# Kernel optimization log

Hardware: AMD Instinct MI355X
Metric: run time of the kernel (lower is better)

Reference implementation:

```python
import jax, jax.numpy as jnp
import numpy as np

B, S, D = 4, 2048, 1024
H = 16
HD = D // H

def setup_inputs() -> dict:
    key = jax.random.key(0)
    ks = jax.random.split(key, 6)
    scale = 0.02
    return {
        "x": jax.random.normal(ks[0], (B, S, D), dtype=jnp.float32),
        "W_q": jax.random.normal(ks[1], (D, D), dtype=jnp.float32) * scale,
        "W_k": jax.random.normal(ks[2], (D, D), dtype=jnp.float32) * scale,
        "W_v": jax.random.normal(ks[3], (D, D), dtype=jnp.float32) * scale,
        "W_o": jax.random.normal(ks[4], (D, D), dtype=jnp.float32) * scale,
        "b_o": jax.random.normal(ks[5], (D,), dtype=jnp.float32) * scale,
    }

def reference(x, W_q, W_k, W_v, W_o, b_o):
    b, s, d = x.shape
    # projections, split heads: [b, h, s, hd]
    q = (x @ W_q).reshape(b, s, H, HD).transpose(0, 2, 1, 3)
    k = (x @ W_k).reshape(b, s, H, HD).transpose(0, 2, 1, 3)
    v = (x @ W_v).reshape(b, s, H, HD).transpose(0, 2, 1, 3)
    scores = jnp.einsum('bhqd,bhkd->bhqk', q, k)
    causal = jnp.triu(jnp.ones((s, s), dtype=bool), k=1)
    scores = jnp.where(causal, -jnp.inf, scores)
    # module divides by sqrt(hd) after masking; -inf stays -inf
    attn = jax.nn.softmax(scores / jnp.sqrt(jnp.float32(HD)), axis=-1)
    ctx = jnp.einsum('bhqk,bhkd->bhqd', attn, v)
    ctx = ctx.transpose(0, 2, 1, 3).reshape(b, s, d)
    return ctx @ W_o + b_o
```

## Files before the change

### kernel.cpp

```cpp
#include <hip/hip_runtime.h>
#include <hip/hip_bf16.h>
#include <math.h>

typedef __attribute__((ext_vector_type(8))) short bf16x8;
typedef __attribute__((ext_vector_type(4))) float f32x4;
typedef unsigned short u16;
typedef __hip_bfloat16 HB;

#define B_ 4
#define S_ 2048
#define D_ 1024
#define H_ 16
#define HD_ 64

__device__ __forceinline__ u16 f2b(float f) {
  HB h = __float2bfloat16(f);
  return *reinterpret_cast<u16*>(&h);
}
__device__ __forceinline__ void store1(HB* p, float v) { *p = __float2bfloat16(v); }
__device__ __forceinline__ void store1(float* p, float v) { *p = v; }

__device__ __forceinline__ void glds16(const u16* g, u16* l) {
  __builtin_amdgcn_global_load_lds(
      (const __attribute__((address_space(1))) void*)g,
      (__attribute__((address_space(3))) void*)l, 16, 0, 0);
}

__global__ __launch_bounds__(256) void cast_x(const float* __restrict__ xin,
                                              u16* __restrict__ xout) {
  const long i0 = ((long)blockIdx.x * 256 + threadIdx.x) * 8;
  bf16x8 r;
#pragma unroll
  for (int j = 0; j < 8; ++j) r[j] = (short)f2b(xin[i0 + j]);
  *(bf16x8*)(xout + i0) = r;
}

__global__ __launch_bounds__(256) void transpose_w(
    const float* __restrict__ w0, const float* __restrict__ w1,
    const float* __restrict__ w2, const float* __restrict__ w3,
    u16* __restrict__ out) {
  __shared__ __align__(16) u16 T[64 * 72];
  const float* Ws[4] = {w0, w1, w2, w3};
  const float* W = Ws[blockIdx.z];
  u16* Wt = out + (long)blockIdx.z * (1 << 20);
  const int t = threadIdx.x;
  const int r = t >> 3;
  const int c8 = (t & 7) * 8;
#pragma unroll
  for (int it = 0; it < 2; ++it) {
    const int row = blockIdx.y * 64 + it * 32 + r;
    const float* src = W + (long)row * D_ + blockIdx.x * 64 + c8;
#pragma unroll
    for (int j = 0; j < 8; ++j) T[(c8 + j) * 72 + it * 32 + r] = f2b(src[j]);
  }
  __syncthreads();
#pragma unroll
  for (int it = 0; it < 2; ++it) {
    const int row = it * 32 + r;
    bf16x8 v = *(const bf16x8*)(&T[row * 72 + c8]);
    *(bf16x8*)(Wt + (long)(blockIdx.x * 64 + row) * D_ + blockIdx.y * 64 + c8) = v;
  }
}

template <typename OT>
__global__ __launch_bounds__(256) void gemm_bt128(
    const u16* __restrict__ A, const u16* __restrict__ BTb, long bt_stride,
    OT* __restrict__ Cb, long c_stride, const float* __restrict__ bias,
    u16* __restrict__ vt, int scale_q, int M, int N, int K) {
  const u16* BT = BTb + (long)blockIdx.z * bt_stride;
  OT* C = Cb + (long)blockIdx.z * c_stride;

  __shared__ __align__(16) u16 As[128 * 32];
  __shared__ __align__(16) u16 Bs[128 * 32];

  const int tid = threadIdx.x;
  const int w = tid >> 6, lane = tid & 63;
  const int qr = lane & 15, quad = lane >> 4;
  const int wm = w >> 1, wn = w & 1;

  const long rowA0 = (long)blockIdx.y * 128;
  const long rowB0 = (long)blockIdx.x * 128;

  const int sr = lane >> 2;
  const int sc8 = ((lane & 3) ^ ((lane >> 3) & 3)) * 8;
  const long arow = rowA0 + w * 16 + sr;
  const long brow = rowB0 + w * 16 + sr;
  u16* asd0 = As + (w * 16) * 32;
  u16* asd1 = As + (64 + w * 16) * 32;
  u16* bsd0 = Bs + (w * 16) * 32;
  u16* bsd1 = Bs + (64 + w * 16) * 32;

  f32x4 acc[4][4] = {};

  for (int k0 = 0; k0 < K; k0 += 32) {
    __syncthreads();
    glds16(A + arow * K + k0 + sc8, asd0);
    glds16(A + (arow + 64) * K + k0 + sc8, asd1);
    glds16(BT + brow * K + k0 + sc8, bsd0);
    glds16(BT + (brow + 64) * K + k0 + sc8, bsd1);
    __syncthreads();

    bf16x8 af[4], bf[4];
#pragma unroll
    for (int ms = 0; ms < 4; ++ms) {
      const int m = wm * 64 + ms * 16 + qr;
      af[ms] = *(const bf16x8*)(&As[m * 32 + ((quad ^ ((m >> 1) & 3)) * 8)]);
    }
#pragma unroll
    for (int ns = 0; ns < 4; ++ns) {
      const int n = wn * 64 + ns * 16 + qr;
      bf[ns] = *(const bf16x8*)(&Bs[n * 32 + ((quad ^ ((n >> 1) & 3)) * 8)]);
    }

#pragma unroll
    for (int ms = 0; ms < 4; ++ms)
#pragma unroll
      for (int ns = 0; ns < 4; ++ns)
        acc[ms][ns] = __builtin_amdgcn_mfma_f32_16x16x32_bf16(
            af[ms], bf[ns], acc[ms][ns], 0, 0, 0);
  }

  if (vt && blockIdx.z == 2) {
#pragma unroll
    for (int ns = 0; ns < 4; ++ns) {
      const int col = (int)rowB0 + wn * 64 + ns * 16 + qr;
#pragma unroll
      for (int ms = 0; ms < 4; ++ms) {
        const long row = rowA0 + wm * 64 + ms * 16 + quad * 4;
        const long b = row >> 11, s = row & 2047;
        ushort4 pk;
        pk.x = f2b(acc[ms][ns][0]); pk.y = f2b(acc[ms][ns][1]);
        pk.z = f2b(acc[ms][ns][2]); pk.w = f2b(acc[ms][ns][3]);
        *(ushort4*)(vt + ((b * H_ + (col >> 6)) * HD_ + (col & 63)) * S_ + s) = pk;
      }
    }
    return;
  }

  const float qs = (scale_q && blockIdx.z == 0) ? 0.125f : 1.f;
#pragma unroll
  for (int ns = 0; ns < 4; ++ns) {
    const long col = rowB0 + wn * 64 + ns * 16 + qr;
    const float bv = bias ? bias[col] : 0.f;
#pragma unroll
    for (int ms = 0; ms < 4; ++ms) {
      const long row = rowA0 + wm * 64 + ms * 16 + quad * 4;
#pragma unroll
      for (int r = 0; r < 4; ++r)
        store1(&C[(row + r) * (long)N + col], acc[ms][ns][r] * qs + bv);
    }
  }
}

__global__ __launch_bounds__(256) void attn4(
    const u16* __restrict__ Q, const u16* __restrict__ Kg,
    const u16* __restrict__ Vt, u16* __restrict__ ctx) {
  __shared__ __align__(16) u16 KV[2][2][64 * 64];
  __shared__ __align__(16) u16 Pl[4][2][16 * 72];

  const int tid = threadIdx.x;
  const int w = tid >> 6, lane = tid & 63;
  const int qr = lane & 15, quad = lane >> 4;
  const int bh = blockIdx.x;
  const int b = bh >> 4, h = bh & 15;

  const long baseQK = ((long)b * S_) * D_ + h * HD_;
  const long baseVt = (long)bh * HD_ * S_;

  const int sr8 = lane >> 3;
  const int sc8 = ((lane & 7) ^ sr8) * 8;

  const int tiles2[2] = {(int)blockIdx.y, 15 - (int)blockIdx.y};

#pragma unroll
  for (int ti = 0; ti < 2; ++ti) {
    const int q0 = tiles2[ti] * 128;
    const int qbase = q0 + w * 32;

    bf16x8 aq[2][2];
#pragma unroll
    for (int i = 0; i < 2; ++i) {
      const u16* qp_ = Q + baseQK + (long)(qbase + i * 16 + qr) * D_;
      aq[i][0] = *(const bf16x8*)(qp_ + quad * 8);
      aq[i][1] = *(const bf16x8*)(qp_ + 32 + quad * 8);
    }

    float l_i[2][4] = {};
    f32x4 o[2][4] = {};

    const int nkt = q0 / 64 + 2;

#pragma unroll
    for (int t = 0; t < 2; ++t) {
      const int r = t * 32 + w * 8 + sr8;
      glds16(Kg + baseQK + (long)r * D_ + sc8, &KV[0][0][(t * 32 + w * 8) * 64]);
      glds16(Vt + baseVt + (long)r * S_ + sc8, &KV[0][1][(t * 32 + w * 8) * 64]);
    }

    for (int kt = 0; kt < nkt; ++kt) {
      const int kbase = kt * 64;
      const int buf = kt & 1;

      __syncthreads();

      if (kt + 1 < nkt) {
        const int nb = kbase + 64;
#pragma unroll
        for (int t = 0; t < 2; ++t) {
          const int r = t * 32 + w * 8 + sr8;
          glds16(Kg + baseQK + (long)(nb + r) * D_ + sc8,
                 &KV[buf ^ 1][0][(t * 32 + w * 8) * 64]);
          glds16(Vt + baseVt + (long)r * S_ + nb + sc8,
                 &KV[buf ^ 1][1][(t * 32 + w * 8) * 64]);
        }
      }

      const u16* Ksb = KV[buf][0];
      const u16* Vsb = KV[buf][1];

      bf16x8 kf[4][2];
#pragma unroll
      for (int ns = 0; ns < 4; ++ns) {
        const int row = ns * 16 + qr;
        kf[ns][0] = *(const bf16x8*)(&Ksb[row * 64 + ((quad ^ (row & 7)) * 8)]);
        kf[ns][1] =
            *(const bf16x8*)(&Ksb[row * 64 + (((4 + quad) ^ (row & 7)) * 8)]);
      }

      f32x4 s[2][4] = {};
#pragma unroll
      for (int i = 0; i < 2; ++i)
#pragma unroll
        for (int ns = 0; ns < 4; ++ns) {
          s[i][ns] = __builtin_amdgcn_mfma_f32_16x16x32_bf16(
              aq[i][0], kf[ns][0], s[i][ns], 0, 0, 0);
          s[i][ns] = __builtin_amdgcn_mfma_f32_16x16x32_bf16(
              aq[i][1], kf[ns][1], s[i][ns], 0, 0, 0);
        }

#pragma unroll
      for (int i = 0; i < 2; ++i) {
        if (kbase + 64 > qbase + i * 16) {
          const int qrow = qbase + i * 16 + quad * 4;
#pragma unroll
          for (int ns = 0; ns < 4; ++ns) {
            const int kcol = kbase + ns * 16 + qr;
#pragma unroll
            for (int r = 0; r < 4; ++r)
              if (kcol > qrow + r) s[i][ns][r] = -1.0e30f;
          }
        }
      }

#pragma unroll
      for (int i = 0; i < 2; ++i) {
        float psum[4] = {};
#pragma unroll
        for (int ns = 0; ns < 4; ++ns)
#pragma unroll
          for (int r = 0; r < 4; ++r) {
            const float p = __expf(s[i][ns][r]);
            psum[r] += p;
            Pl[w][i][(quad * 4 + r) * 72 + ns * 16 + qr] = f2b(p);
          }
#pragma unroll
        for (int r = 0; r < 4; ++r) {
          float ps = psum[r];
#pragma unroll
          for (int off = 1; off < 16; off <<= 1) ps += __shfl_xor(ps, off, 64);
          l_i[i][r] += ps;
        }
      }

      bf16x8 vf[4][2];
#pragma unroll
      for (int ns = 0; ns < 4; ++ns) {
        const int row = ns * 16 + qr;
        vf[ns][0] = *(const bf16x8*)(&Vsb[row * 64 + ((quad ^ (row & 7)) * 8)]);
        vf[ns][1] =
            *(const bf16x8*)(&Vsb[row * 64 + (((4 + quad) ^ (row & 7)) * 8)]);
      }

#pragma unroll
      for (int i = 0; i < 2; ++i) {
        bf16x8 pf0 = *(const bf16x8*)(&Pl[w][i][qr * 72 + quad * 8]);
        bf16x8 pf1 = *(const bf16x8*)(&Pl[w][i][qr * 72 + 32 + quad * 8]);
#pragma unroll
        for (int ns = 0; ns < 4; ++ns) {
          o[i][ns] = __builtin_amdgcn_mfma_f32_16x16x32_bf16(pf0, vf[ns][0],
                                                             o[i][ns], 0, 0, 0);
          o[i][ns] = __builtin_amdgcn_mfma_f32_16x16x32_bf16(pf1, vf[ns][1],
                                                             o[i][ns], 0, 0, 0);
        }
      }
    }

#pragma unroll
    for (int i = 0; i < 2; ++i)
#pragma unroll
      for (int r = 0; r < 4; ++r) {
        const float inv = 1.f / l_i[i][r];
        const long row = qbase + i * 16 + quad * 4 + r;
#pragma unroll
        for (int ns = 0; ns < 4; ++ns)
          ctx[((long)b * S_ + row) * D_ + h * HD_ + ns * 16 + qr] =
              f2b(o[i][ns][r] * inv);
      }
  }
}

extern "C" void kernel_launch(void* const* d_in, const int* in_sizes, int n_in,
                              void* d_out, int out_size, void* d_ws,
                              size_t ws_size, hipStream_t stream) {
  const float* x  = (const float*)d_in[0];
  const float* Wq = (const float*)d_in[1];
  const float* Wk = (const float*)d_in[2];
  const float* Wv = (const float*)d_in[3];
  const float* Wo = (const float*)d_in[4];
  const float* bo = (const float*)d_in[5];

  u16* ws = (u16*)d_ws;
  u16* xb  = ws;
  u16* Wt  = xb + 8388608l;
  u16* Qb  = Wt + 4l * 1048576;
  u16* Kb  = Qb + 8388608l;
  u16* Vb  = Kb + 8388608l;
  u16* ctx = Qb;

  cast_x<<<4096, 256, 0, stream>>>(x, xb);

  transpose_w<<<dim3(16, 16, 4), 256, 0, stream>>>(Wq, Wk, Wv, Wo, Wt);

  gemm_bt128<HB><<<dim3(8, 64, 3), 256, 0, stream>>>(
      xb, Wt, 1048576l, (HB*)Qb, 8388608l, nullptr, Vb, 1, 8192, 1024, 1024);

  attn4<<<dim3(64, 8), 256, 0, stream>>>(Qb, Kb, Vb, ctx);

  gemm_bt128<float><<<dim3(8, 64, 1), 256, 0, stream>>>(
      ctx, Wt + 3l * 1048576, 0, (float*)d_out, 0, bo, nullptr, 0,
      8192, 1024, 1024);
}
```

Baseline: 305.8 us.

## Transpose score MFMA layout, fold log2e into Q scale, use exp2

Swaps the MFMA operands so each lane holds four consecutive key columns of one query row. Probabilities can then be packed as ushort4 into a swizzled 64-wide LDS tile instead of scalar bf16 stores. The row-sum reduction shrinks to two cross-quad shuffles with one accumulator per row tile, plus a final shuffle to fetch the denominator. The Q scale now folds in log2(e), so the softmax can use the hardware exp2 instruction instead of __expf. It still does no max subtraction, which relies on scores staying bounded, and the extra final shuffles add a little work.

After: 282.8 us. 7.5% less time.

```diff
diff --git a/kernel.cpp b/kernel.cpp
--- a/kernel.cpp
+++ b/kernel.cpp
@@ -19,6 +19,14 @@
 }
 __device__ __forceinline__ void store1(HB* p, float v) { *p = __float2bfloat16(v); }
 __device__ __forceinline__ void store1(float* p, float v) { *p = v; }
+
+__device__ __forceinline__ float fexp2(float x) {
+#if __has_builtin(__builtin_amdgcn_exp2f)
+  return __builtin_amdgcn_exp2f(x);
+#else
+  return exp2f(x);
+#endif
+}
 
 __device__ __forceinline__ void glds16(const u16* g, u16* l) {
   __builtin_amdgcn_global_load_lds(
@@ -137,7 +145,7 @@
     return;
   }
 
-  const float qs = (scale_q && blockIdx.z == 0) ? 0.125f : 1.f;
+  const float qs = (scale_q && blockIdx.z == 0) ? 0.18033688011112042f : 1.f;
 #pragma unroll
   for (int ns = 0; ns < 4; ++ns) {
     const long col = rowB0 + wn * 64 + ns * 16 + qr;
@@ -152,11 +160,11 @@
   }
 }
 
-__global__ __launch_bounds__(256) void attn4(
+__global__ __launch_bounds__(256) void attn5(
     const u16* __restrict__ Q, const u16* __restrict__ Kg,
     const u16* __restrict__ Vt, u16* __restrict__ ctx) {
   __shared__ __align__(16) u16 KV[2][2][64 * 64];
-  __shared__ __align__(16) u16 Pl[4][2][16 * 72];
+  __shared__ __align__(16) u16 Pl[4][16 * 64];
 
   const int tid = threadIdx.x;
   const int w = tid >> 6, lane = tid & 63;
@@ -185,7 +193,7 @@
       aq[i][1] = *(const bf16x8*)(qp_ + 32 + quad * 8);
     }
 
-    float l_i[2][4] = {};
+    float li[2] = {};
     f32x4 o[2][4] = {};
 
     const int nkt = q0 / 64 + 2;
@@ -233,42 +241,22 @@
 #pragma unroll
         for (int ns = 0; ns < 4; ++ns) {
           s[i][ns] = __builtin_amdgcn_mfma_f32_16x16x32_bf16(
-              aq[i][0], kf[ns][0], s[i][ns], 0, 0, 0);
+              kf[ns][0], aq[i][0], s[i][ns], 0, 0, 0);
           s[i][ns] = __builtin_amdgcn_mfma_f32_16x16x32_bf16(
-              aq[i][1], kf[ns][1], s[i][ns], 0, 0, 0);
+              kf[ns][1], aq[i][1], s[i][ns], 0, 0, 0);
         }
 
 #pragma unroll
       for (int i = 0; i < 2; ++i) {
         if (kbase + 64 > qbase + i * 16) {
-          const int qrow = qbase + i * 16 + quad * 4;
+          const int qrow = qbase + i * 16 + qr;
 #pragma unroll
           for (int ns = 0; ns < 4; ++ns) {
-            const int kcol = kbase + ns * 16 + qr;
+            const int kc = kbase + ns * 16 + quad * 4;
 #pragma unroll
             for (int r = 0; r < 4; ++r)
-              if (kcol > qrow + r) s[i][ns][r] = -1.0e30f;
+              if (kc + r > qrow) s[i][ns][r] = -1.0e30f;
           }
-        }
-      }
-
-#pragma unroll
-      for (int i = 0; i < 2; ++i) {
-        float psum[4] = {};
-#pragma unroll
-        for (int ns = 0; ns < 4; ++ns)
-#pragma unroll
-          for (int r = 0; r < 4; ++r) {
-            const float p = __expf(s[i][ns][r]);
-            psum[r] += p;
-            Pl[w][i][(quad * 4 + r) * 72 + ns * 16 + qr] = f2b(p);
-          }
-#pragma unroll
-        for (int r = 0; r < 4; ++r) {
-          float ps = psum[r];
-#pragma unroll
-          for (int off = 1; off < 16; off <<= 1) ps += __shfl_xor(ps, off, 64);
-          l_i[i][r] += ps;
         }
       }
 
@@ -283,8 +271,27 @@
 
 #pragma unroll
       for (int i = 0; i < 2; ++i) {
-        bf16x8 pf0 = *(const bf16x8*)(&Pl[w][i][qr * 72 + quad * 8]);
-        bf16x8 pf1 = *(const bf16x8*)(&Pl[w][i][qr * 72 + 32 + quad * 8]);
+        float ps = 0.f;
+#pragma unroll
+        for (int ns = 0; ns < 4; ++ns) {
+          const float p0 = fexp2(s[i][ns][0]);
+          const float p1 = fexp2(s[i][ns][1]);
+          const float p2 = fexp2(s[i][ns][2]);
+          const float p3 = fexp2(s[i][ns][3]);
+          ps += (p0 + p1) + (p2 + p3);
+          ushort4 pk;
+          pk.x = f2b(p0); pk.y = f2b(p1); pk.z = f2b(p2); pk.w = f2b(p3);
+          *(ushort4*)(&Pl[w][qr * 64 +
+                             (((2 * ns + (quad >> 1)) ^ (qr & 7)) * 8) +
+                             (quad & 1) * 4]) = pk;
+        }
+        ps += __shfl_xor(ps, 16, 64);
+        ps += __shfl_xor(ps, 32, 64);
+        li[i] += ps;
+
+        bf16x8 pf0 = *(const bf16x8*)(&Pl[w][qr * 64 + ((quad ^ (qr & 7)) * 8)]);
+        bf16x8 pf1 =
+            *(const bf16x8*)(&Pl[w][qr * 64 + (((4 + quad) ^ (qr & 7)) * 8)]);
 #pragma unroll
         for (int ns = 0; ns < 4; ++ns) {
           o[i][ns] = __builtin_amdgcn_mfma_f32_16x16x32_bf16(pf0, vf[ns][0],
@@ -299,7 +306,7 @@
     for (int i = 0; i < 2; ++i)
 #pragma unroll
       for (int r = 0; r < 4; ++r) {
-        const float inv = 1.f / l_i[i][r];
+        const float inv = 1.f / __shfl(li[i], quad * 4 + r, 64);
         const long row = qbase + i * 16 + quad * 4 + r;
 #pragma unroll
         for (int ns = 0; ns < 4; ++ns)
@@ -334,7 +341,7 @@
   gemm_bt128<HB><<<dim3(8, 64, 3), 256, 0, stream>>>(
       xb, Wt, 1048576l, (HB*)Qb, 8388608l, nullptr, Vb, 1, 8192, 1024, 1024);
 
-  attn4<<<dim3(64, 8), 256, 0, stream>>>(Qb, Kb, Vb, ctx);
+  attn5<<<dim3(64, 8), 256, 0, stream>>>(Qb, Kb, Vb, ctx);
 
   gemm_bt128<float><<<dim3(8, 64, 1), 256, 0, stream>>>(
       ctx, Wt + 3l * 1048576, 0, (float*)d_out, 0, bo, nullptr, 0,
```
